# Kernel optimization log

Hardware: AMD Instinct MI355X
Metric: run time of the kernel (lower is better)

The kernel has to match this reference:

```python
import jax, jax.numpy as jnp
import numpy as np

B, S, D, E, K = 2, 2048, 1024, 8, 2
DFF = 4 * D


def setup_inputs() -> dict:
    key = jax.random.key(0)
    ks = jax.random.split(key, 7)
    scale = 0.02
    return {
        "x": jax.random.normal(ks[0], (B, S, D), dtype=jnp.float32),
        "W1": jax.random.normal(ks[1], (E, D, DFF), dtype=jnp.float32) * scale,
        "b1": jnp.zeros((E, DFF), dtype=jnp.float32),
        "W2": jax.random.normal(ks[2], (E, DFF, D), dtype=jnp.float32) * scale,
        "b2": jnp.zeros((E, D), dtype=jnp.float32),
        "Wg": jax.random.normal(ks[3], (D, E), dtype=jnp.float32) * scale,
        "bg": jnp.zeros((E,), dtype=jnp.float32),
    }


def reference(x, W1, b1, W2, b2, Wg, bg):
    num_experts = W1.shape[0]
    # Gating: top-k logits -> softmax over the k selected experts
    gate_logits = jnp.einsum("bsd,de->bse", x, Wg) + bg          # [B,S,E]
    topk_w, topk_i = jax.lax.top_k(gate_logits, K)               # [B,S,K]
    topk_w = jax.nn.softmax(topk_w, axis=-1)
    # Per-expert combine weight (sum of routed weights, 0 if not routed)
    w = jnp.sum(
        jax.nn.one_hot(topk_i, num_experts, dtype=x.dtype) * topk_w[..., None],
        axis=-2,
    )                                                            # [B,S,E]
    # Faithful to original: every expert runs its full FFN over all tokens,
    # then outputs are masked by routing weights and summed.
    h = jax.nn.gelu(jnp.einsum("bsd,edf->bsef", x, W1) + b1, approximate=False)
    out = jnp.einsum("bsef,efd,bse->bsd", h, W2, w)
    out = out + jnp.einsum("bse,ed->bsd", w, b2)
    return out
```

## Files before the change

### kernel.cpp

```cpp
#include <hip/hip_runtime.h>
#include <math.h>

#define TOK 4096
#define D 1024
#define DFF 4096
#define NE 8
#define CAP 4096
#define YSLOTS 9216
#define NTMAX 72
#define GTOK 16

typedef _Float16 half4v __attribute__((ext_vector_type(4)));
typedef _Float16 half8v __attribute__((ext_vector_type(8)));
typedef float f32x4 __attribute__((ext_vector_type(4)));

#define GLOAD16(gp, lp) __builtin_amdgcn_global_load_lds( \
    (const __attribute__((address_space(1))) void*)(gp),  \
    (__attribute__((address_space(3))) void*)(lp), 16, 0, 0)

__device__ __forceinline__ float fast_gelu(float v) {
    float u = 0.7978845608f * (v + 0.044715f * v * v * v);
    float au = fabsf(u);
    float t = __expf(-2.f * au);
    float th = (1.f - t) / (1.f + t);
    th = u < 0.f ? -th : th;
    return 0.5f * v * (1.f + th);
}


__global__ void k_gate(const float* __restrict__ x, const float* __restrict__ Wg,
                       const float* __restrict__ bg, int* __restrict__ counts,
                       int* __restrict__ tk_e, float* __restrict__ tk_w,
                       int* __restrict__ tk_pos, int* __restrict__ tok_list,
                       _Float16* __restrict__ xh) {
    __shared__ int s_e[2 * GTOK];
    __shared__ int s_rank[2 * GTOK];
    __shared__ int s_base[NE];
    int wid = threadIdx.x >> 6, lane = threadIdx.x & 63;
    int tbase = blockIdx.x * GTOK;

    for (int i = 0; i < 4; ++i) {
        int tl = wid * 4 + i;
        int t = tbase + tl;
        const float* xr = x + (size_t)t * D;
        float a[NE];
#pragma unroll
        for (int e = 0; e < NE; ++e) a[e] = 0.f;
        for (int d = lane; d < D; d += 64) {
            float xv = xr[d];
            const float4 w0 = *(const float4*)(Wg + d * NE);
            const float4 w1 = *(const float4*)(Wg + d * NE + 4);
            a[0] += xv * w0.x; a[1] += xv * w0.y; a[2] += xv * w0.z; a[3] += xv * w0.w;
            a[4] += xv * w1.x; a[5] += xv * w1.y; a[6] += xv * w1.z; a[7] += xv * w1.w;
        }
#pragma unroll
        for (int j = 0; j < 2; ++j) {
            int ch = j * 64 + lane;
            float4 va = *(const float4*)(xr + ch * 8);
            float4 vb = *(const float4*)(xr + ch * 8 + 4);
            half8v h;
            h[0] = (_Float16)va.x; h[1] = (_Float16)va.y; h[2] = (_Float16)va.z; h[3] = (_Float16)va.w;
            h[4] = (_Float16)vb.x; h[5] = (_Float16)vb.y; h[6] = (_Float16)vb.z; h[7] = (_Float16)vb.w;
            *(half8v*)(xh + (size_t)t * D + ch * 8) = h;
        }
#pragma unroll
        for (int m = 1; m < 64; m <<= 1) {
#pragma unroll
            for (int e = 0; e < NE; ++e) a[e] += __shfl_xor(a[e], m, 64);
        }
        if (lane == 0) {
#pragma unroll
            for (int e = 0; e < NE; ++e) a[e] += bg[e];
            int i0 = 0;
#pragma unroll
            for (int e = 1; e < NE; ++e) if (a[e] > a[i0]) i0 = e;
            int i1 = (i0 == 0) ? 1 : 0;
#pragma unroll
            for (int e = 0; e < NE; ++e) if (e != i0 && a[e] > a[i1]) i1 = e;
            float ee = expf(a[i1] - a[i0]);
            float w0 = 1.f / (1.f + ee);
            float w1 = ee / (1.f + ee);
            tk_e[t * 2] = i0; tk_e[t * 2 + 1] = i1;
            tk_w[t * 2] = w0; tk_w[t * 2 + 1] = w1;
            s_e[tl * 2] = i0; s_e[tl * 2 + 1] = i1;
        }
    }
    __syncthreads();
    int tid = threadIdx.x;
    if (tid < 2 * GTOK) {
        int ei = s_e[tid];
        int r = 0;
#pragma unroll
        for (int j = 0; j < 2 * GTOK; ++j) r += (j < tid && s_e[j] == ei) ? 1 : 0;
        s_rank[tid] = r;
    } else if (tid >= 64 && tid < 64 + NE) {
        int e = tid - 64;
        int cnt = 0;
#pragma unroll
        for (int j = 0; j < 2 * GTOK; ++j) cnt += (s_e[j] == e) ? 1 : 0;
        s_base[e] = cnt ? atomicAdd(&counts[e], cnt) : 0;
    }
    __syncthreads();
    if (tid < 2 * GTOK) {
        int ei = s_e[tid];
        int t = tbase + (tid >> 1);
        int pos = s_base[ei] + s_rank[tid];
        tok_list[ei * CAP + pos] = t;
        tk_pos[t * 2 + (tid & 1)] = pos;
    }
}

__global__ void k_prep(const int* __restrict__ counts, int* __restrict__ offs) {
    int o = 0;
    for (int e = 0; e < NE; ++e) { offs[e] = o; o += (counts[e] + 127) & ~127; }
    offs[NE] = o;
}

__global__ void k_tr2(const float* __restrict__ W1, const float* __restrict__ W2,
                      _Float16* __restrict__ W1t, _Float16* __restrict__ W2t) {
    int y = blockIdx.y;
    const float* S; _Float16* T; int R, C, r0, c0;
    if (y < 8) {
        S = W1 + (size_t)y * D * DFF; T = W1t + (size_t)y * DFF * D; R = D; C = DFF;
        c0 = (blockIdx.x & 63) * 64; r0 = (blockIdx.x >> 6) * 128;
    } else {
        S = W2 + (size_t)(y - 8) * DFF * D; T = W2t + (size_t)(y - 8) * D * DFF; R = DFF; C = D;
        c0 = (blockIdx.x & 15) * 64; r0 = (blockIdx.x >> 4) * 128;
    }
    __shared__ float tile_t[64][129];
    int tid = threadIdx.x;
    int cl = tid & 63;
    int rl = (tid >> 6) * 32;
#pragma unroll
    for (int k = 0; k < 32; ++k) {
        int r = rl + k;
        tile_t[cl][r] = S[(size_t)(r0 + r) * C + c0 + cl];
    }
    __syncthreads();
    int j = tid & 7;
#pragma unroll
    for (int p = 0; p < 2; ++p) {
        int c = p * 32 + (tid >> 3);
#pragma unroll
        for (int i = 0; i < 2; ++i) {
            int rb = i * 64 + j * 8;
            half8v h;
#pragma unroll
            for (int jj = 0; jj < 8; ++jj) h[jj] = (_Float16)tile_t[c][rb + jj];
            *(half8v*)(T + (size_t)(c0 + c) * R + r0 + rb) = h;
        }
    }
}

__global__ __launch_bounds__(256, 4)
void k_ffn1(const _Float16* __restrict__ xh, const _Float16* __restrict__ W1t,
            const float* __restrict__ b1, const int* __restrict__ counts,
            const int* __restrict__ offs, const int* __restrict__ tok_list,
            _Float16* __restrict__ H) {
    int T = blockIdx.y;
    if (T * 128 >= offs[NE]) return;
    int e = 0;
#pragma unroll
    for (int k = 1; k < NE; ++k) if (offs[k] <= T * 128) e = k;
    int row0 = T * 128 - offs[e];
    int n_e = counts[e];
    int bx = blockIdx.x;

    __shared__ __align__(16) char smem[34816];
    _Float16* As = (_Float16*)smem;
    _Float16* Bs = (_Float16*)(smem + 16384);
    int* s_tok = (int*)(smem + 32768);

    int tid = threadIdx.x, lane = tid & 63, wid = tid >> 6;
    if (tid < 128) {
        int m = row0 + tid;
        s_tok[tid] = tok_list[e * CAP + (m < n_e ? m : n_e - 1)];
    }
    __syncthreads();

    int srow = lane >> 3, u = lane & 7;
    int wm = (wid >> 1) * 64, wn = (wid & 1) * 64;
    int cl = lane & 15, g = lane >> 4;
    int v8 = u ^ srow;
    int rbase = wid * 32 + srow;

    const _Float16* Abase = W1t + (size_t)e * DFF * D + (size_t)(bx * 128) * D + v8 * 8;
    const _Float16* bsrc[4];
#pragma unroll
    for (int i = 0; i < 4; ++i)
        bsrc[i] = xh + (size_t)s_tok[rbase + i * 8] * D + v8 * 8;

    f32x4 acc[4][4];
#pragma unroll
    for (int i = 0; i < 4; ++i)
#pragma unroll
        for (int j = 0; j < 4; ++j) acc[i][j] = (f32x4)0.f;

    for (int kt = 0; kt < D; kt += 64) {
#pragma unroll
        for (int i = 0; i < 4; ++i)
            GLOAD16(Abase + (size_t)(rbase + i * 8) * D + kt, As + (wid * 4 + i) * 512);
#pragma unroll
        for (int i = 0; i < 4; ++i)
            GLOAD16(bsrc[i] + kt, Bs + (wid * 4 + i) * 512);
        __syncthreads();
#pragma unroll
        for (int ks = 0; ks < 2; ++ks) {
            half8v aF[4], bF[4];
            int vv = ((ks * 4 + g) ^ (cl & 7)) * 8;
#pragma unroll
            for (int fm = 0; fm < 4; ++fm)
                aF[fm] = *(const half8v*)(As + (wm + fm * 16 + cl) * 64 + vv);
#pragma unroll
            for (int fn = 0; fn < 4; ++fn)
                bF[fn] = *(const half8v*)(Bs + (wn + fn * 16 + cl) * 64 + vv);
#pragma unroll
            for (int fm = 0; fm < 4; ++fm)
#pragma unroll
                for (int fn = 0; fn < 4; ++fn)
                    acc[fm][fn] = __builtin_amdgcn_mfma_f32_16x16x32_f16(aF[fm], bF[fn], acc[fm][fn], 0, 0, 0);
        }
        __syncthreads();
    }

    _Float16* Tile = (_Float16*)smem;
#pragma unroll
    for (int fm = 0; fm < 4; ++fm) {
        int featl = wm + fm * 16 + g * 4;
        float4 bv = *(const float4*)(b1 + e * DFF + bx * 128 + featl);
        float bb[4] = {bv.x, bv.y, bv.z, bv.w};
#pragma unroll
        for (int fn = 0; fn < 4; ++fn) {
            int sl = wn + fn * 16 + cl;
            half4v hv;
#pragma unroll
            for (int j = 0; j < 4; ++j) {
                float vv2 = acc[fm][fn][j] + bb[j];
                hv[j] = (_Float16)fast_gelu(vv2);
            }
            *(half4v*)(&Tile[sl * 136 + featl]) = hv;
        }
    }
    __syncthreads();
#pragma unroll
    for (int p = 0; p < 8; ++p) {
        int r = p * 16 + (tid >> 4);
        int c8 = (tid & 15) * 8;
        if (row0 + r < n_e)
            *(half8v*)(H + (size_t)(T * 128 + r) * DFF + bx * 128 + c8) =
                *(const half8v*)(&Tile[r * 136 + c8]);
    }
}

__global__ __launch_bounds__(256, 4)
void k_ffn2(const _Float16* __restrict__ H, const _Float16* __restrict__ W2t,
            const int* __restrict__ counts, const int* __restrict__ offs,
            _Float16* __restrict__ Yh) {
    int wg = blockIdx.x;
    int xcd = wg & 7, j = wg >> 3;
    int bx = j & 7;
    int tl = (j >> 3) % 9;
    int kh = j / 72;
    int T = xcd * 9 + tl;
    if (T * 128 >= offs[NE]) return;
    int e = 0;
#pragma unroll
    for (int k = 1; k < NE; ++k) if (offs[k] <= T * 128) e = k;
    int row0 = T * 128 - offs[e];
    int n_e = counts[e];

    __shared__ __align__(16) char smem[34816];
    _Float16* As = (_Float16*)smem;
    _Float16* Bs = (_Float16*)(smem + 16384);

    int tid = threadIdx.x, lane = tid & 63, wid = tid >> 6;
    int srow = lane >> 3, u = lane & 7;
    int wm = (wid >> 1) * 64, wn = (wid & 1) * 64;
    int cl = lane & 15, g = lane >> 4;
    int v8 = u ^ srow;
    int rbase = wid * 32 + srow;

    const _Float16* Abase = W2t + (size_t)e * D * DFF + (size_t)(bx * 128) * DFF + v8 * 8;
    const _Float16* Bbase = H + (size_t)(T * 128) * DFF + v8 * 8;

    f32x4 acc[4][4];
#pragma unroll
    for (int i = 0; i < 4; ++i)
#pragma unroll
        for (int j2 = 0; j2 < 4; ++j2) acc[i][j2] = (f32x4)0.f;

    int kt0 = kh * 2048, kt1 = kt0 + 2048;
    for (int kt = kt0; kt < kt1; kt += 64) {
#pragma unroll
        for (int i = 0; i < 4; ++i)
            GLOAD16(Abase + (size_t)(rbase + i * 8) * DFF + kt, As + (wid * 4 + i) * 512);
#pragma unroll
        for (int i = 0; i < 4; ++i)
            GLOAD16(Bbase + (size_t)(rbase + i * 8) * DFF + kt, Bs + (wid * 4 + i) * 512);
        __syncthreads();
#pragma unroll
        for (int ks = 0; ks < 2; ++ks) {
            half8v aF[4], bF[4];
            int vv = ((ks * 4 + g) ^ (cl & 7)) * 8;
#pragma unroll
            for (int fm = 0; fm < 4; ++fm)
                aF[fm] = *(const half8v*)(As + (wm + fm * 16 + cl) * 64 + vv);
#pragma unroll
            for (int fn = 0; fn < 4; ++fn)
                bF[fn] = *(const half8v*)(Bs + (wn + fn * 16 + cl) * 64 + vv);
#pragma unroll
            for (int fm = 0; fm < 4; ++fm)
#pragma unroll
                for (int fn = 0; fn < 4; ++fn)
                    acc[fm][fn] = __builtin_amdgcn_mfma_f32_16x16x32_f16(aF[fm], bF[fn], acc[fm][fn], 0, 0, 0);
        }
        __syncthreads();
    }

    _Float16* Tile = (_Float16*)smem;
#pragma unroll
    for (int fm = 0; fm < 4; ++fm) {
        int dl = wm + fm * 16 + g * 4;
#pragma unroll
        for (int fn = 0; fn < 4; ++fn) {
            int sl = wn + fn * 16 + cl;
            half4v hv;
#pragma unroll
            for (int j2 = 0; j2 < 4; ++j2) hv[j2] = (_Float16)acc[fm][fn][j2];
            *(half4v*)(&Tile[sl * 136 + dl]) = hv;
        }
    }
    __syncthreads();
#pragma unroll
    for (int p = 0; p < 8; ++p) {
        int r = p * 16 + (tid >> 4);
        int c8 = (tid & 15) * 8;
        if (row0 + r < n_e)
            *(half8v*)(Yh + ((size_t)kh * YSLOTS + T * 128 + r) * D + bx * 128 + c8) =
                *(const half8v*)(&Tile[r * 136 + c8]);
    }
}

__global__ void k_comb(const int* __restrict__ tk_e, const float* __restrict__ tk_w,
                       const int* __restrict__ tk_pos, const int* __restrict__ offs,
                       const _Float16* __restrict__ Yh, const float* __restrict__ b2,
                       float* __restrict__ out) {
    int idx = blockIdx.x * 256 + threadIdx.x;
    int t = idx >> 8;
    int d = (idx & 255) * 4;
    int e0 = tk_e[2 * t], e1 = tk_e[2 * t + 1];
    float w0 = tk_w[2 * t], w1 = tk_w[2 * t + 1];
    size_t s0 = offs[e0] + tk_pos[2 * t];
    size_t s1 = offs[e1] + tk_pos[2 * t + 1];
    half4v y00 = *(const half4v*)(Yh + s0 * D + d);
    half4v y01 = *(const half4v*)(Yh + ((size_t)YSLOTS + s0) * D + d);
    half4v y10 = *(const half4v*)(Yh + s1 * D + d);
    half4v y11 = *(const half4v*)(Yh + ((size_t)YSLOTS + s1) * D + d);
    float4 b20 = *(const float4*)(b2 + e0 * D + d);
    float4 b21 = *(const float4*)(b2 + e1 * D + d);
    float4 r;
    r.x = w0 * ((float)y00[0] + (float)y01[0] + b20.x) + w1 * ((float)y10[0] + (float)y11[0] + b21.x);
    r.y = w0 * ((float)y00[1] + (float)y01[1] + b20.y) + w1 * ((float)y10[1] + (float)y11[1] + b21.y);
    r.z = w0 * ((float)y00[2] + (float)y01[2] + b20.z) + w1 * ((float)y10[2] + (float)y11[2] + b21.z);
    r.w = w0 * ((float)y00[3] + (float)y01[3] + b20.w) + w1 * ((float)y10[3] + (float)y11[3] + b21.w);
    *(float4*)(out + (size_t)t * D + d) = r;
}

extern "C" void kernel_launch(void* const* d_in, const int* in_sizes, int n_in,
                              void* d_out, int out_size, void* d_ws, size_t ws_size,
                              hipStream_t stream) {
    const float* x  = (const float*)d_in[0];
    const float* W1 = (const float*)d_in[1];
    const float* b1 = (const float*)d_in[2];
    const float* W2 = (const float*)d_in[3];
    const float* b2 = (const float*)d_in[4];
    const float* Wg = (const float*)d_in[5];
    const float* bg = (const float*)d_in[6];
    float* out = (float*)d_out;

    char* ws = (char*)d_ws;
    int*   counts   = (int*)(ws);
    int*   offs     = (int*)(ws + 64);
    int*   tk_e     = (int*)(ws + 256);
    float* tk_w     = (float*)(ws + 33024);
    int*   tk_pos   = (int*)(ws + 65792);
    int*   tok_list = (int*)(ws + 98560);
    _Float16* xh    = (_Float16*)(ws + (1ull << 20));
    _Float16* W1t   = (_Float16*)(ws + (10ull << 20));
    _Float16* Yh    = (_Float16*)(ws + (10ull << 20));
    _Float16* W2t   = (_Float16*)(ws + (74ull << 20));
    _Float16* H     = (_Float16*)(ws + (138ull << 20));

    hipMemsetAsync(counts, 0, 64, stream);
    k_gate<<<TOK / GTOK, 256, 0, stream>>>(x, Wg, bg, counts, tk_e, tk_w, tk_pos, tok_list, xh);
    k_prep<<<1, 1, 0, stream>>>(counts, offs);
    k_tr2<<<dim3(512, 16), 256, 0, stream>>>(W1, W2, W1t, W2t);
    k_ffn1<<<dim3(DFF / 128, NTMAX, 1), 256, 0, stream>>>(xh, W1t, b1, counts, offs, tok_list, H);
    k_ffn2<<<8 * 144, 256, 0, stream>>>(H, W2t, counts, offs, Yh);
    k_comb<<<(TOK * D / 4) / 256, 256, 0, stream>>>(tk_e, tk_w, tk_pos, offs, Yh, b2, out);
}
```

Before: 321.6 us.

## Fold weight transposes into gate and FFN1 kernels to overlap work

Removes the separate k_tr2 launch. The W1 transpose/fp16 conversion now runs as extra blocks appended to the gating kernel, and the W2 transpose runs as extra blocks appended to the FFN1 GEMM kernel. The intent is to hide the memory-bound transpose work behind compute-bound or latency-bound kernels and save a launch. In exchange, the transpose blocks compete for CUs with the GEMM and gate blocks. The fused kernels also inherit larger shared-memory and launch-bound constraints.

```diff
diff --git a/kernel.cpp b/kernel.cpp
--- a/kernel.cpp
+++ b/kernel.cpp
@@ -27,17 +27,56 @@
     return 0.5f * v * (1.f + th);
 }
 
-
-__global__ void k_gate(const float* __restrict__ x, const float* __restrict__ Wg,
-                       const float* __restrict__ bg, int* __restrict__ counts,
-                       int* __restrict__ tk_e, float* __restrict__ tk_w,
-                       int* __restrict__ tk_pos, int* __restrict__ tok_list,
-                       _Float16* __restrict__ xh) {
-    __shared__ int s_e[2 * GTOK];
-    __shared__ int s_rank[2 * GTOK];
-    __shared__ int s_base[NE];
-    int wid = threadIdx.x >> 6, lane = threadIdx.x & 63;
-    int tbase = blockIdx.x * GTOK;
+__device__ __forceinline__ void tr_tile(const float* __restrict__ S,
+                                        _Float16* __restrict__ T,
+                                        int R, int C, int r0, int c0,
+                                        char* smem, int tid) {
+    float (*tile_t)[129] = (float(*)[129])smem;
+    int cl = tid & 63;
+    int rl = (tid >> 6) * 32;
+#pragma unroll
+    for (int k = 0; k < 32; ++k) {
+        int r = rl + k;
+        tile_t[cl][r] = S[(size_t)(r0 + r) * C + c0 + cl];
+    }
+    __syncthreads();
+    int j = tid & 7;
+#pragma unroll
+    for (int p = 0; p < 2; ++p) {
+        int c = p * 32 + (tid >> 3);
+#pragma unroll
+        for (int i = 0; i < 2; ++i) {
+            int rb = i * 64 + j * 8;
+            half8v h;
+#pragma unroll
+            for (int jj = 0; jj < 8; ++jj) h[jj] = (_Float16)tile_t[c][rb + jj];
+            *(half8v*)(T + (size_t)(c0 + c) * R + r0 + rb) = h;
+        }
+    }
+}
+
+
+__global__ void k_gate_trw1(const float* __restrict__ x, const float* __restrict__ Wg,
+                            const float* __restrict__ bg, int* __restrict__ counts,
+                            int* __restrict__ tk_e, float* __restrict__ tk_w,
+                            int* __restrict__ tk_pos, int* __restrict__ tok_list,
+                            _Float16* __restrict__ xh,
+                            const float* __restrict__ W1, _Float16* __restrict__ W1t) {
+    __shared__ __align__(16) char smem[33024];
+    int bid = blockIdx.x;
+    int tid = threadIdx.x;
+    if (bid >= 256) {
+        int t = bid - 256;
+        int e = t >> 9, xx = t & 511;
+        tr_tile(W1 + (size_t)e * D * DFF, W1t + (size_t)e * DFF * D,
+                D, DFF, (xx >> 6) * 128, (xx & 63) * 64, smem, tid);
+        return;
+    }
+    int* s_e = (int*)smem;
+    int* s_rank = (int*)(smem + 128);
+    int* s_base = (int*)(smem + 256);
+    int wid = tid >> 6, lane = tid & 63;
+    int tbase = bid * GTOK;
 
     for (int i = 0; i < 4; ++i) {
         int tl = wid * 4 + i;
@@ -86,7 +125,6 @@
         }
     }
     __syncthreads();
-    int tid = threadIdx.x;
     if (tid < 2 * GTOK) {
         int ei = s_e[tid];
         int r = 0;
@@ -116,62 +154,36 @@
     offs[NE] = o;
 }
 
-__global__ void k_tr2(const float* __restrict__ W1, const float* __restrict__ W2,
-                      _Float16* __restrict__ W1t, _Float16* __restrict__ W2t) {
-    int y = blockIdx.y;
-    const float* S; _Float16* T; int R, C, r0, c0;
-    if (y < 8) {
-        S = W1 + (size_t)y * D * DFF; T = W1t + (size_t)y * DFF * D; R = D; C = DFF;
-        c0 = (blockIdx.x & 63) * 64; r0 = (blockIdx.x >> 6) * 128;
-    } else {
-        S = W2 + (size_t)(y - 8) * DFF * D; T = W2t + (size_t)(y - 8) * D * DFF; R = DFF; C = D;
-        c0 = (blockIdx.x & 15) * 64; r0 = (blockIdx.x >> 4) * 128;
-    }
-    __shared__ float tile_t[64][129];
+__global__ __launch_bounds__(256, 4)
+void k_ffn1_trw2(const _Float16* __restrict__ xh, const _Float16* __restrict__ W1t,
+                 const float* __restrict__ b1, const int* __restrict__ counts,
+                 const int* __restrict__ offs, const int* __restrict__ tok_list,
+                 _Float16* __restrict__ H,
+                 const float* __restrict__ W2, _Float16* __restrict__ W2t) {
+    __shared__ __align__(16) char smem[34816];
+    int bid = blockIdx.x;
     int tid = threadIdx.x;
-    int cl = tid & 63;
-    int rl = (tid >> 6) * 32;
-#pragma unroll
-    for (int k = 0; k < 32; ++k) {
-        int r = rl + k;
-        tile_t[cl][r] = S[(size_t)(r0 + r) * C + c0 + cl];
-    }
-    __syncthreads();
-    int j = tid & 7;
-#pragma unroll
-    for (int p = 0; p < 2; ++p) {
-        int c = p * 32 + (tid >> 3);
-#pragma unroll
-        for (int i = 0; i < 2; ++i) {
-            int rb = i * 64 + j * 8;
-            half8v h;
-#pragma unroll
-            for (int jj = 0; jj < 8; ++jj) h[jj] = (_Float16)tile_t[c][rb + jj];
-            *(half8v*)(T + (size_t)(c0 + c) * R + r0 + rb) = h;
-        }
-    }
-}
-
-__global__ __launch_bounds__(256, 4)
-void k_ffn1(const _Float16* __restrict__ xh, const _Float16* __restrict__ W1t,
-            const float* __restrict__ b1, const int* __restrict__ counts,
-            const int* __restrict__ offs, const int* __restrict__ tok_list,
-            _Float16* __restrict__ H) {
-    int T = blockIdx.y;
+    if (bid >= 2304) {
+        int t = bid - 2304;
+        int e = t >> 9, xx = t & 511;
+        tr_tile(W2 + (size_t)e * DFF * D, W2t + (size_t)e * D * DFF,
+                DFF, D, (xx >> 4) * 128, (xx & 15) * 64, smem, tid);
+        return;
+    }
+    int T = bid >> 5;
     if (T * 128 >= offs[NE]) return;
     int e = 0;
 #pragma unroll
     for (int k = 1; k < NE; ++k) if (offs[k] <= T * 128) e = k;
     int row0 = T * 128 - offs[e];
     int n_e = counts[e];
-    int bx = blockIdx.x;
-
-    __shared__ __align__(16) char smem[34816];
+    int bx = bid & 31;
+
     _Float16* As = (_Float16*)smem;
     _Float16* Bs = (_Float16*)(smem + 16384);
     int* s_tok = (int*)(smem + 32768);
 
-    int tid = threadIdx.x, lane = tid & 63, wid = tid >> 6;
+    int lane = tid & 63, wid = tid >> 6;
     if (tid < 128) {
         int m = row0 + tid;
         s_tok[tid] = tok_list[e * CAP + (m < n_e ? m : n_e - 1)];
@@ -392,10 +404,11 @@
     _Float16* H     = (_Float16*)(ws + (138ull << 20));
 
     hipMemsetAsync(counts, 0, 64, stream);
-    k_gate<<<TOK / GTOK, 256, 0, stream>>>(x, Wg, bg, counts, tk_e, tk_w, tk_pos, tok_list, xh);
+    k_gate_trw1<<<256 + 4096, 256, 0, stream>>>(x, Wg, bg, counts, tk_e, tk_w, tk_pos,
+                                                tok_list, xh, W1, W1t);
     k_prep<<<1, 1, 0, stream>>>(counts, offs);
-    k_tr2<<<dim3(512, 16), 256, 0, stream>>>(W1, W2, W1t, W2t);
-    k_ffn1<<<dim3(DFF / 128, NTMAX, 1), 256, 0, stream>>>(xh, W1t, b1, counts, offs, tok_list, H);
+    k_ffn1_trw2<<<2304 + 4096, 256, 0, stream>>>(xh, W1t, b1, counts, offs, tok_list,
+                                                 H, W2, W2t);
     k_ffn2<<<8 * 144, 256, 0, stream>>>(H, W2t, counts, offs, Yh);
     k_comb<<<(TOK * D / 4) / 256, 256, 0, stream>>>(tk_e, tk_w, tk_pos, offs, Yh, b2, out);
 }
```

After: 297.6 us. 7.5% less time.
